# Optimization experiments

Measured on AMD Instinct MI355X. Metric: run time of the kernel, lower is better.

Reference implementation:

```python
import jax, jax.numpy as jnp
import numpy as np

HEADS = 8; KVH = 4; HD = 64; MULT = 2; DIFF = 1; DIM = 512; K = 3
LAMBDA_INIT = 0.2          # 0.8 - 0.6*exp(-0.3*layer_idx), layer_idx=0, affine=False
EPS = 1e-8
ROPE_CONST = 10000.0


def conv2d(x, w):
    # SAME padding (=1) for k=3, stride 1, zeros padding mode, no bias
    return jax.lax.conv_general_dilated(x, w, (1, 1), [(1, 1), (1, 1)],
                                        dimension_numbers=('NCHW', 'OIHW', 'NCHW'))


def rope(x):
    # x: [B, S, h, D]; rotate interleaved pairs (torch view_as_complex layout)
    D = x.shape[-1]; S = x.shape[1]
    theta = 1.0 / (ROPE_CONST ** (jnp.arange(0, D, 2, dtype=jnp.float32) / D))
    ang = jnp.arange(S, dtype=jnp.float32)[:, None] * theta[None, :]      # [S, D/2]
    cos = jnp.cos(ang)[None, :, None, :]
    sin = jnp.sin(ang)[None, :, None, :]
    xr = x.reshape(*x.shape[:-1], D // 2, 2)
    x0, x1 = xr[..., 0], xr[..., 1]
    out = jnp.stack([x0 * cos - x1 * sin, x0 * sin + x1 * cos], axis=-1)
    return out.reshape(x.shape)


def setup_inputs() -> dict:
    key = jax.random.key(0)
    ks = jax.random.split(key, 10)
    conv_std = 1.0 / np.sqrt(DIM * K * K)
    x = jax.random.normal(ks[0], (1, 2, DIM, 64, 64), jnp.float32)
    cross = jax.random.normal(ks[1], (1, 2, DIM, 32, 32), jnp.float32)
    wq = jax.random.normal(ks[2], (HEADS * HD * MULT, DIM, K, K), jnp.float32) * conv_std
    wk = jax.random.normal(ks[3], (KVH * HD * MULT, DIM, K, K), jnp.float32) * conv_std
    wv = jax.random.normal(ks[4], (KVH * HD, DIM, K, K), jnp.float32) * conv_std
    wo = jax.random.normal(ks[5], (DIM, DIM, K, K), jnp.float32) * conv_std
    # lambda params scaled to keep exp(sum over head_dim) numerically sane
    lam_q1 = jax.random.normal(ks[6], (HEADS, HD, DIFF), jnp.float32) * 0.05
    lam_q2 = jax.random.normal(ks[7], (HEADS, HD, DIFF), jnp.float32) * 0.05
    lam_k1 = jax.random.normal(ks[8], (HEADS, HD, DIFF), jnp.float32) * 0.05
    lam_k2 = jax.random.normal(ks[9], (HEADS, HD, DIFF), jnp.float32) * 0.05
    return {'x': x, 'cross': cross, 'wq': wq, 'wk': wk, 'wv': wv, 'wo': wo,
            'lam_q1': lam_q1, 'lam_q2': lam_q2, 'lam_k1': lam_k1, 'lam_k2': lam_k2}


def reference(x, cross, wq, wk, wv, wo, lam_q1, lam_q2, lam_k1, lam_k2):
    g, b, c, H, W = x.shape
    _, _, _, Hc, Wc = cross.shape
    B = g * b; Sq = H * W; Sk = Hc * Wc
    xb = x.reshape(B, c, H, W)
    cb = cross.reshape(B, c, Hc, Wc)
    # conv QKV projections
    q = conv2d(xb, wq)                     # [B, heads*HD*MULT, H, W]
    k = conv2d(cb, wk)                     # [B, KVH*HD*MULT, Hc, Wc]
    v = conv2d(cb, wv)                     # [B, KVH*HD, Hc, Wc]
    # convert: channels are head-major -> [B, S, heads, HD*mult]
    q = q.reshape(B, HEADS, HD * MULT, Sq).transpose(0, 3, 1, 2)
    k = k.reshape(B, KVH, HD * MULT, Sk).transpose(0, 3, 1, 2)
    v = v.reshape(B, KVH, HD, Sk).transpose(0, 3, 1, 2)
    # RoPE over flattened pixel positions, rotating full HD*MULT per head
    q = rope(q)
    k = rope(k)
    # grouped-query: repeat kv heads
    rep = HEADS // KVH
    k = jnp.repeat(k, rep, axis=2)         # [B, Sk, heads, HD*MULT]
    v = jnp.repeat(v, rep, axis=2)         # [B, Sk, heads, HD]
    # split into 1+DIFF score components
    qm = q.reshape(B, Sq, HEADS, MULT, HD)
    km = k.reshape(B, Sk, HEADS, MULT, HD)
    scale = 1.0 / np.sqrt(HD)
    scores = jnp.einsum('bqhmd,bkhmd->bhmqk', qm, km) * scale
    attn = jax.nn.softmax(scores, axis=-1)               # [B, h, MULT, Sq, Sk]
    # differential lambda: ((exp(sum q1*k1) - exp(sum q2*k2)) + init) * (-1)^i
    signs = (-1.0) ** jnp.arange(1, DIFF + 1, dtype=jnp.float32)   # [DIFF]
    lam = (jnp.exp(jnp.sum(lam_q1 * lam_k1, axis=-2))
           - jnp.exp(jnp.sum(lam_q2 * lam_k2, axis=-2)) + LAMBDA_INIT) * signs  # [h, DIFF]
    combined = attn[:, :, 0] + jnp.einsum('hm,bhmqk->bhqk', lam, attn[:, :, 1:])
    out = jnp.einsum('bhqk,bkhd->bqhd', combined, v)     # [B, Sq, h, HD]
    # per-head RMSNorm (affine=False) then post-attention shift
    out = out * jax.lax.rsqrt(jnp.mean(out * out, axis=-1, keepdims=True) + EPS)
    out = out * (1.0 - LAMBDA_INIT)
    # revert to image layout and output conv
    out = out.reshape(B, Sq, HEADS * HD).transpose(0, 2, 1).reshape(B, c, H, W)
    out = conv2d(out, wo)
    return out.reshape(g, b, c, H, W)
```

## Files before the change

### kernel.cpp

```cpp
#include <hip/hip_runtime.h>


typedef __attribute__((ext_vector_type(8))) short short8;
typedef __attribute__((ext_vector_type(4))) float f32x4;
typedef unsigned short us;

__device__ __forceinline__ float bf2f(us u) {
  union { unsigned int i; float f; } v; v.i = ((unsigned int)u) << 16; return v.f;
}
__device__ __forceinline__ us f2bf(float f) {
  union { float f; unsigned int i; } v; v.f = f;
  unsigned int x = v.i;
  return (us)((x + 0x7fffu + ((x >> 16) & 1u)) >> 16);
}

typedef __attribute__((address_space(3))) unsigned int as3_uint;
typedef const __attribute__((address_space(1))) unsigned int as1_uint;
__device__ __forceinline__ void gload16(const us* g, us* l) {
  __builtin_amdgcn_global_load_lds((as1_uint*)g, (as3_uint*)l, 16, 0, 0);
}
__device__ __forceinline__ unsigned int cvt_pk_bf16(float a, float b) {
  unsigned int r;
  asm("v_cvt_pk_bf16_f32 %0, %1, %2" : "=v"(r) : "v"(a), "v"(b));
  return r;
}
__device__ __forceinline__ float fast_exp2(float x) {
  float r;
  asm("v_exp_f32 %0, %1" : "=v"(r) : "v"(x));
  return r;
}
__device__ __forceinline__ void fsincos(float ang, float* sn, float* cs) {
  float r = ang * 0.15915494309f;
  r = r - floorf(r);
  float s, c;
  asm("v_sin_f32 %0, %1" : "=v"(s) : "v"(r));
  asm("v_cos_f32 %0, %1" : "=v"(c) : "v"(r));
  *sn = s; *cs = c;
}

__device__ __forceinline__ void transpose_body(
    const float* __restrict__ in, us* __restrict__ outT,
    int b, int y, int ci0, int H, int W, int logW) {
  const int C = 512;
  int padW = W + 2, Ppad = (H + 2) * padW;
  __shared__ float tile[64][65];
  int nt = W * 64;
  for (int idx = threadIdx.x; idx < nt; idx += 256) {
    int ci = idx >> logW, x = idx & (W - 1);
    tile[ci][x] = in[(((size_t)b * C + ci0 + ci) * H + y) * W + x];
  }
  __syncthreads();
  int nt2 = W * 32;
  for (int idx = threadIdx.x; idx < nt2; idx += 256) {
    int px = idx >> 5, c2 = idx & 31;
    unsigned int val = (unsigned int)f2bf(tile[c2 * 2][px]) |
                       ((unsigned int)f2bf(tile[c2 * 2 + 1][px]) << 16);
    *(unsigned int*)(outT + ((size_t)b * Ppad + (size_t)(y + 1) * padW + (px + 1)) * C +
                     ci0 + c2 * 2) = val;
  }
}

__global__ __launch_bounds__(256) void prep_all(
    const float* __restrict__ x, const float* __restrict__ cross,
    const float* __restrict__ wq, const float* __restrict__ wk,
    const float* __restrict__ wv, const float* __restrict__ wo,
    const float* __restrict__ lq1, const float* __restrict__ lq2,
    const float* __restrict__ lk1, const float* __restrict__ lk2,
    us* __restrict__ xpadT, us* __restrict__ cpadT, us* __restrict__ apad,
    us* __restrict__ oq, us* __restrict__ ok, us* __restrict__ ov,
    us* __restrict__ oo, float* __restrict__ lam) {
  int bid = blockIdx.x, tid = threadIdx.x;
  if (bid < 326) {
    int g = bid * 4 + (tid >> 6);
    int t = tid & 63;
    us* base; int W, b, i;
    if (g < 520)      { base = xpadT; W = 64; b = g >= 260; i = g - b * 260; }
    else if (g < 784) { base = cpadT; W = 32; int gg = g - 520; b = gg >= 132; i = gg - b * 132; }
    else              { base = apad; W = 64; int gg = g - 784; b = gg >= 260; i = gg - b * 260; }
    int padW = W + 2, nb = 2 * padW;
    int yy, xx;
    if (i < padW)    { yy = 0; xx = i; }
    else if (i < nb) { yy = W + 1; xx = i - padW; }
    else             { int j = i - nb; yy = 1 + (j >> 1); xx = (j & 1) * (W + 1); }
    size_t p = ((size_t)b * padW * padW + (size_t)yy * padW + xx) * 512 + t * 8;
    *(int4*)(base + p) = make_int4(0, 0, 0, 0);
  } else if (bid < 1350) {
    int i = bid - 326;
    transpose_body(x, xpadT, i >> 9, (i >> 3) & 63, (i & 7) * 64, 64, 64, 6);
  } else if (bid < 1862) {
    int i = bid - 1350;
    transpose_body(cross, cpadT, i >> 8, (i >> 3) & 31, (i & 7) * 64, 32, 32, 5);
  } else if (bid < 4166) {
    int blk = bid - 1862;
    const float* src; us* dst; int Cout, co;
    if (blk < 1024)      { src = wq; dst = oq; Cout = 1024; co = blk; }
    else if (blk < 1536) { src = wk; dst = ok; Cout = 512;  co = blk - 1024; }
    else if (blk < 1792) { src = wv; dst = ov; Cout = 256;  co = blk - 1536; }
    else                 { src = wo; dst = oo; Cout = 512;  co = blk - 1792; }
    __shared__ us l[4608];
    const float* s0 = src + (size_t)co * 4608;
#pragma unroll
    for (int k = 0; k < 18; ++k) { int i = k * 256 + tid; l[i] = f2bf(s0[i]); }
    __syncthreads();
#pragma unroll
    for (int k = 0; k < 9; ++k) {
      int j = k * 256 + tid;
      int t = j >> 8, c2 = j & 255;
      unsigned int val = (unsigned int)l[(c2 * 2) * 9 + t] |
                         ((unsigned int)l[(c2 * 2 + 1) * 9 + t] << 16);
      *(unsigned int*)(dst + (size_t)t * Cout * 512 + (size_t)co * 512 + c2 * 2) = val;
    }
  } else {
    int h = tid >> 5, d = tid & 31;
    float s1 = lq1[h * 64 + d] * lk1[h * 64 + d] +
               lq1[h * 64 + d + 32] * lk1[h * 64 + d + 32];
    float s2 = lq2[h * 64 + d] * lk2[h * 64 + d] +
               lq2[h * 64 + d + 32] * lk2[h * 64 + d + 32];
    for (int m = 16; m; m >>= 1) {
      s1 += __shfl_xor(s1, m);
      s2 += __shfl_xor(s2, m);
    }
    if (d == 0) lam[h] = -(expf(s1) - expf(s2) + 0.2f);
  }
}

__global__ __launch_bounds__(256) void conv128_fwd(
    const us* __restrict__ inT, const us* __restrict__ wp,
    us* __restrict__ out, int Cout) {
  __shared__ __align__(16) us sh[2][2][128][64];
  int bid = blockIdx.x;
  int v = (bid & 7) * 64 + (bid >> 3);
  int pxt = v & 31, cot = (v >> 5) & 7, b = v >> 8;
  int p0 = pxt * 128, co0 = cot * 128;
  int tid = threadIdx.x;
  int wave = tid >> 6, lane = tid & 63, l15 = lane & 15, hi4 = lane >> 4;
  int wr = wave >> 1, wc = wave & 1;
  f32x4 acc[4][4];
#pragma unroll
  for (int m = 0; m < 4; ++m)
#pragma unroll
    for (int n = 0; n < 4; ++n) acc[m][n] = (f32x4){0.f, 0.f, 0.f, 0.f};

  int arow[4], brow[4];
#pragma unroll
  for (int c = 0; c < 4; ++c) {
    int row = c * 32 + (tid >> 3);
    int g = (tid & 7) ^ (row & 7);
    int px = p0 + row;
    int y = px >> 6, x = px & 63;
    arow[c] = (y * 66 + x) * 512 + g * 8;
    brow[c] = (co0 + row) * 512 + g * 8;
  }
  int aoff[4][2], boff[4][2];
#pragma unroll
  for (int m = 0; m < 4; ++m)
#pragma unroll
    for (int ks = 0; ks < 2; ++ks) {
      int ra = wr * 64 + m * 16 + l15;
      int rb = wc * 64 + m * 16 + l15;
      aoff[m][ks] = ra * 64 + (((ks * 4 + hi4) ^ (l15 & 7)) * 8);
      boff[m][ks] = rb * 64 + (((ks * 4 + hi4) ^ (l15 & 7)) * 8);
    }
  const us* abase = inT + (size_t)b * 66 * 66 * 512;

  auto stage = [&](int buf, int s) {
    int tn = s >> 3, ci = (s & 7) << 6;
    int ky = (tn * 11) >> 5, kx = tn - ky * 3;
    const us* as = abase + (ky * 66 + kx) * 512 + ci;
    const us* bs = wp + (size_t)tn * Cout * 512 + ci;
    us* la = &sh[buf][0][0][0];
    us* lb = &sh[buf][1][0][0];
#pragma unroll
    for (int c = 0; c < 4; ++c) {
      gload16(as + arow[c], la + c * 2048 + wave * 512);
      gload16(bs + brow[c], lb + c * 2048 + wave * 512);
    }
  };

  stage(0, 0);
  __syncthreads();
  for (int s = 0; s < 72; ++s) {
    int cur = s & 1;
    if (s < 71) stage(cur ^ 1, s + 1);
    const us* la = &sh[cur][0][0][0];
    const us* lb = &sh[cur][1][0][0];
#pragma unroll
    for (int ks = 0; ks < 2; ++ks) {
      short8 af[4], bf[4];
#pragma unroll
      for (int m = 0; m < 4; ++m) af[m] = *(const short8*)(la + aoff[m][ks]);
#pragma unroll
      for (int n = 0; n < 4; ++n) bf[n] = *(const short8*)(lb + boff[n][ks]);
#pragma unroll
      for (int m = 0; m < 4; ++m)
#pragma unroll
        for (int n = 0; n < 4; ++n)
          acc[m][n] = __builtin_amdgcn_mfma_f32_16x16x32_bf16(af[m], bf[n], acc[m][n], 0, 0, 0);
    }
    __syncthreads();
  }
  int par = lane & 1;
#pragma unroll
  for (int n = 0; n < 4; ++n) {
    int co = co0 + wc * 64 + n * 16 + l15;
    int j = (co & 127) >> 1;
    float th = exp2f(-(float)j * 0.20762050593f);
    float sth, cth;
    fsincos(th, &sth, &cth);
#pragma unroll
    for (int m = 0; m < 4; ++m) {
      int pxb = p0 + wr * 64 + m * 16 + hi4 * 4;
      float s0, c0;
      fsincos((float)pxb * th, &s0, &c0);
#pragma unroll
      for (int r = 0; r < 4; ++r) {
        float xv = acc[m][n][r];
        float ov = __shfl_xor(xv, 1);
        float y = par ? fmaf(ov, s0, xv * c0) : fmaf(xv, c0, -ov * s0);
        out[((size_t)b * 4096 + (pxb + r)) * Cout + co] = f2bf(y);
        float c1 = c0 * cth - s0 * sth;
        s0 = fmaf(c0, sth, s0 * cth);
        c0 = c1;
      }
    }
  }
}

template <int TRANS_OUT, int ROPE>
__device__ __forceinline__ void conv64_body(
    const us* __restrict__ inT, const us* __restrict__ wp,
    us* __restrict__ out, int Cout, int logCoT, int bid, int ngrid, us* sh) {
  int nchunk = ngrid >> 3;
  int v = (bid & 7) * nchunk + (bid >> 3);
  int yt = v & 15;
  int cot = (v >> 4) & ((1 << logCoT) - 1);
  int b = v >> (4 + logCoT);
  int p0 = yt * 64, co0 = cot * 64;
  const int W = 32, logW = 5, padW = 34, HW = 1024;
  int tid = threadIdx.x;
  int wave = tid >> 6, lane = tid & 63, l15 = lane & 15, hi4 = lane >> 4;
  f32x4 acc[4];
#pragma unroll
  for (int i = 0; i < 4; ++i) acc[i] = (f32x4){0.f, 0.f, 0.f, 0.f};

  int arow[2], brow[2];
#pragma unroll
  for (int c = 0; c < 2; ++c) {
    int row = (wave * 2 + c) * 8 + (lane >> 3);
    int g = (lane & 7) ^ (row & 7);
    int px = p0 + row;
    int y = px >> logW, x = px & (W - 1);
    arow[c] = (y * padW + x) * 512 + g * 8;
    brow[c] = (co0 + row) * 512 + g * 8;
  }
  int gb[2];
#pragma unroll
  for (int ks = 0; ks < 2; ++ks) gb[ks] = ((ks * 4 + hi4) ^ (l15 & 7)) * 8;

  const us* abase = inT + (size_t)b * padW * padW * 512;

  auto stage = [&](int buf, int s) {
    int tn = s >> 3, ci = (s & 7) << 6;
    int ky = (tn * 11) >> 5, kx = tn - ky * 3;
    const us* as = abase + (ky * padW + kx) * 512 + ci;
    const us* bs = wp + (size_t)tn * Cout * 512 + ci;
    us* la = sh + buf * 8192;
    us* lb = la + 4096;
#pragma unroll
    for (int c = 0; c < 2; ++c) {
      gload16(as + arow[c], la + (wave * 2 + c) * 512);
      gload16(bs + brow[c], lb + (wave * 2 + c) * 512);
    }
  };

  stage(0, 0);
  __syncthreads();
  for (int s = 0; s < 72; ++s) {
    int cur = s & 1;
    if (s < 71) stage(cur ^ 1, s + 1);
    const us* la = sh + cur * 8192;
    const us* lb = la + 4096;
#pragma unroll
    for (int ks = 0; ks < 2; ++ks) {
      short8 bf = *(const short8*)(lb + (16 * wave + l15) * 64 + gb[ks]);
#pragma unroll
      for (int i = 0; i < 4; ++i) {
        short8 af = *(const short8*)(la + (i * 16 + l15) * 64 + gb[ks]);
        acc[i] = __builtin_amdgcn_mfma_f32_16x16x32_bf16(af, bf, acc[i], 0, 0, 0);
      }
    }
    __syncthreads();
  }
  if (ROPE) {
    int co = co0 + 16 * wave + l15;
    int j = (co & 127) >> 1;
    float th = exp2f(-(float)j * 0.20762050593f);
    float sth, cth;
    fsincos(th, &sth, &cth);
    int par = lane & 1;
#pragma unroll
    for (int i = 0; i < 4; ++i) {
      int pxb = p0 + i * 16 + hi4 * 4;
      float s0, c0;
      fsincos((float)pxb * th, &s0, &c0);
#pragma unroll
      for (int r = 0; r < 4; ++r) {
        float xv = acc[i][r];
        float ov = __shfl_xor(xv, 1);
        float y = par ? fmaf(ov, s0, xv * c0) : fmaf(xv, c0, -ov * s0);
        out[((size_t)b * HW + (pxb + r)) * Cout + co] = f2bf(y);
        float c1 = c0 * cth - s0 * sth;
        s0 = fmaf(c0, sth, s0 * cth);
        c0 = c1;
      }
    }
  } else {
#pragma unroll
    for (int i = 0; i < 4; ++i)
#pragma unroll
      for (int r = 0; r < 4; ++r) {
        int px = TRANS_OUT ? (p0 + (hi4 * 4 + r) * 4 + i)
                           : (p0 + i * 16 + hi4 * 4 + r);
        int co = co0 + 16 * wave + l15;
        us val = f2bf(acc[i][r]);
        if (TRANS_OUT)
          out[((size_t)b * Cout + co) * HW + px] = val;
        else
          out[((size_t)b * HW + px) * Cout + co] = val;
      }
  }
}

__global__ __launch_bounds__(256) void conv64_all(
    const us* __restrict__ cpadT, const us* __restrict__ wkp,
    const us* __restrict__ wvp, us* __restrict__ kb, us* __restrict__ vT) {
  __shared__ __align__(16) us sh[2][2][64][64];
  int bid = blockIdx.x;
  if (bid < 256) conv64_body<0, 1>(cpadT, wkp, kb, 512, 3, bid, 256, &sh[0][0][0][0]);
  else           conv64_body<1, 0>(cpadT, wvp, vT, 256, 2, bid - 256, 128, &sh[0][0][0][0]);
}

__global__ __launch_bounds__(256) void conv128_out(
    const us* __restrict__ apad, const us* __restrict__ wp,
    float* __restrict__ out) {
  __shared__ __align__(16) us lds[2][12288];
  int bid = blockIdx.x;
  int v = (bid & 7) * 64 + (bid >> 3);
  int pxt = v & 63, cot = (v >> 6) & 3, b = v >> 8;
  int p0 = pxt * 64, co0 = cot * 128;
  int tid = threadIdx.x;
  int wave = tid >> 6, lane = tid & 63, l15 = lane & 15, hi4 = lane >> 4;
  int wr = wave >> 1, wc = wave & 1;
  f32x4 acc[4][2];
#pragma unroll
  for (int m = 0; m < 4; ++m)
#pragma unroll
    for (int n = 0; n < 2; ++n) acc[m][n] = (f32x4){0.f, 0.f, 0.f, 0.f};

  int arow[4], brow[2];
#pragma unroll
  for (int c = 0; c < 4; ++c) {
    int row = c * 32 + (tid >> 3);
    int g = (tid & 7) ^ (row & 7);
    arow[c] = (co0 + row) * 512 + g * 8;
  }
#pragma unroll
  for (int c = 0; c < 2; ++c) {
    int row = c * 32 + (tid >> 3);
    int g = (tid & 7) ^ (row & 7);
    int px = p0 + row;
    int y = px >> 6, x = px & 63;
    brow[c] = (y * 66 + x) * 512 + g * 8;
  }
  int aoff[4][2], boff[2][2];
#pragma unroll
  for (int m = 0; m < 4; ++m)
#pragma unroll
    for (int ks = 0; ks < 2; ++ks) {
      int ra = wr * 64 + m * 16 + l15;
      aoff[m][ks] = ra * 64 + (((ks * 4 + hi4) ^ (l15 & 7)) * 8);
    }
#pragma unroll
  for (int n = 0; n < 2; ++n)
#pragma unroll
    for (int ks = 0; ks < 2; ++ks) {
      int rb = wc * 32 + n * 16 + l15;
      boff[n][ks] = rb * 64 + (((ks * 4 + hi4) ^ (l15 & 7)) * 8);
    }
  const us* bbase = apad + (size_t)b * 4356 * 512;

  auto stage = [&](int buf, int s) {
    int tn = s >> 3, ci = (s & 7) << 6;
    int ky = (tn * 11) >> 5, kx = tn - ky * 3;
    const us* as = wp + (size_t)tn * 512 * 512 + ci;
    const us* bs = bbase + (ky * 66 + kx) * 512 + ci;
    us* la = &lds[buf][0];
    us* lb = la + 8192;
#pragma unroll
    for (int c = 0; c < 4; ++c)
      gload16(as + arow[c], la + c * 2048 + wave * 512);
#pragma unroll
    for (int c = 0; c < 2; ++c)
      gload16(bs + brow[c], lb + c * 2048 + wave * 512);
  };

  stage(0, 0);
  __syncthreads();
  for (int s = 0; s < 72; ++s) {
    int cur = s & 1;
    if (s < 71) stage(cur ^ 1, s + 1);
    const us* la = &lds[cur][0];
    const us* lb = la + 8192;
#pragma unroll
    for (int ks = 0; ks < 2; ++ks) {
      short8 af[4], bf[2];
#pragma unroll
      for (int m = 0; m < 4; ++m) af[m] = *(const short8*)(la + aoff[m][ks]);
#pragma unroll
      for (int n = 0; n < 2; ++n) bf[n] = *(const short8*)(lb + boff[n][ks]);
#pragma unroll
      for (int m = 0; m < 4; ++m)
#pragma unroll
        for (int n = 0; n < 2; ++n)
          acc[m][n] = __builtin_amdgcn_mfma_f32_16x16x32_bf16(af[m], bf[n], acc[m][n], 0, 0, 0);
    }
    __syncthreads();
  }
#pragma unroll
  for (int m = 0; m < 4; ++m)
#pragma unroll
    for (int n = 0; n < 2; ++n)
#pragma unroll
      for (int r = 0; r < 4; ++r) {
        int co = co0 + wr * 64 + m * 16 + hi4 * 4 + r;
        int px = p0 + wc * 32 + n * 16 + l15;
        out[((size_t)b * 512 + co) * 4096 + px] = acc[m][n][r];
      }
}

__global__ __launch_bounds__(256) void attn_kernel(
    const us* __restrict__ qb, const us* __restrict__ kb,
    const us* __restrict__ vT, const float* __restrict__ lam,
    us* __restrict__ apad) {
  int qt = blockIdx.x, h = blockIdx.y, b = blockIdx.z;
  int kvh = h >> 1;
  int tid = threadIdx.x;
  int wave = tid >> 6, lane = tid & 63, l15 = lane & 15, hi4 = lane >> 4;
  __shared__ __align__(16) us Klds[2][8192];
  __shared__ __align__(16) us Vlds[2][4096];
  __shared__ __align__(16) us Plds[4][16][72];

  int q0 = qt * 128;
  short8 qf[2][2][2];
  {
    const us* qsrc =
        qb + ((size_t)(b * 4096 + q0 + wave * 32 + l15)) * 1024 + h * 128 + hi4 * 8;
#pragma unroll
    for (int mf = 0; mf < 2; ++mf)
#pragma unroll
      for (int m = 0; m < 2; ++m)
#pragma unroll
        for (int ks = 0; ks < 2; ++ks)
          qf[mf][m][ks] = *(const short8*)(qsrc + mf * 16384 + m * 64 + ks * 32);
  }

  float sumd[2][2][4];
  f32x4 accO[2][2][4];
#pragma unroll
  for (int mf = 0; mf < 2; ++mf)
#pragma unroll
    for (int m = 0; m < 2; ++m)
#pragma unroll
      for (int r = 0; r < 4; ++r) {
        sumd[mf][m][r] = 0.f;
        accO[mf][m][r] = (f32x4){0.f, 0.f, 0.f, 0.f};
      }
  float lamh = lam[h];

  const us* kbase0 = kb + (size_t)b * 524288 + kvh * 128;
  const us* vbase0 = vT + ((size_t)(b * 256 + kvh * 64)) * 1024;
  int krow[4], vrow[2];
#pragma unroll
  for (int c = 0; c < 4; ++c) {
    int row = (wave * 4 + c) * 4 + hi4;
    int g = (l15 & 8) | ((l15 & 7) ^ (row & 7));
    krow[c] = row * 512 + g * 8;
  }
#pragma unroll
  for (int c = 0; c < 2; ++c) {
    int row = (wave * 2 + c) * 8 + (lane >> 3);
    int g = (lane & 7) ^ (row & 7);
    vrow[c] = row * 1024 + g * 8;
  }
  int kg0[2], kg1[2], vg[2];
#pragma unroll
  for (int m = 0; m < 2; ++m) {
    kg0[m] = (m * 8 | (hi4 ^ (l15 & 7))) * 8;
    kg1[m] = (m * 8 | ((4 + hi4) ^ (l15 & 7))) * 8;
  }
#pragma unroll
  for (int ks = 0; ks < 2; ++ks) vg[ks] = ((ks * 4 + hi4) ^ (l15 & 7)) * 8;

  auto stage = [&](int buf, int kt2) {
    const us* kk = kbase0 + (size_t)kt2 * 32768;
    const us* vv = vbase0 + kt2 * 64;
#pragma unroll
    for (int c = 0; c < 4; ++c)
      gload16(kk + krow[c], &Klds[buf][(wave * 4 + c) * 512]);
#pragma unroll
    for (int c = 0; c < 2; ++c)
      gload16(vv + vrow[c], &Vlds[buf][(wave * 2 + c) * 512]);
  };

  const float cexp = 0.18033688f;
  stage(0, 0);
  for (int kt = 0; kt < 16; ++kt) {
    int cur = kt & 1;
    if (kt < 15) {
      stage(cur ^ 1, kt + 1);
      asm volatile("s_waitcnt vmcnt(6)" ::: "memory");
    } else {
      asm volatile("s_waitcnt vmcnt(0)" ::: "memory");
    }
    __builtin_amdgcn_s_barrier();
    __builtin_amdgcn_sched_barrier(0);

    short8 vf[2][4];
#pragma unroll
    for (int ks = 0; ks < 2; ++ks)
#pragma unroll
      for (int nf = 0; nf < 4; ++nf)
        vf[ks][nf] = *(const short8*)&Vlds[cur][(nf * 16 + l15) * 64 + vg[ks]];

#pragma unroll
    for (int m = 0; m < 2; ++m) {
      short8 kf[4][2];
#pragma unroll
      for (int nf = 0; nf < 4; ++nf) {
        kf[nf][0] = *(const short8*)&Klds[cur][(nf * 16 + l15) * 128 + kg0[m]];
        kf[nf][1] = *(const short8*)&Klds[cur][(nf * 16 + l15) * 128 + kg1[m]];
      }
#pragma unroll
      for (int mf = 0; mf < 2; ++mf) {
        f32x4 s[4];
        __builtin_amdgcn_s_setprio(1);
#pragma unroll
        for (int nf = 0; nf < 4; ++nf) {
          f32x4 z = (f32x4){0.f, 0.f, 0.f, 0.f};
          z = __builtin_amdgcn_mfma_f32_16x16x32_bf16(qf[mf][m][0], kf[nf][0], z, 0, 0, 0);
          z = __builtin_amdgcn_mfma_f32_16x16x32_bf16(qf[mf][m][1], kf[nf][1], z, 0, 0, 0);
          s[nf] = z;
        }
        __builtin_amdgcn_s_setprio(0);
#pragma unroll
        for (int r = 0; r < 4; ++r) {
          float p0 = fast_exp2(s[0][r] * cexp);
          float p1 = fast_exp2(s[1][r] * cexp);
          float p2 = fast_exp2(s[2][r] * cexp);
          float p3 = fast_exp2(s[3][r] * cexp);
          sumd[mf][m][r] += (p0 + p1) + (p2 + p3);
          unsigned int w0 = cvt_pk_bf16(p0, p1);
          unsigned int w1 = cvt_pk_bf16(p2, p3);
          *(uint2*)&Plds[wave][hi4 * 4 + r][l15 * 4] = make_uint2(w0, w1);
        }
        __builtin_amdgcn_s_setprio(1);
#pragma unroll
        for (int ks = 0; ks < 2; ++ks) {
          short8 pf = *(const short8*)&Plds[wave][l15][ks * 32 + hi4 * 8];
#pragma unroll
          for (int nf = 0; nf < 4; ++nf)
            accO[mf][m][nf] =
                __builtin_amdgcn_mfma_f32_16x16x32_bf16(pf, vf[ks][nf], accO[mf][m][nf], 0, 0, 0);
        }
        __builtin_amdgcn_s_setprio(0);
      }
    }
    asm volatile("s_waitcnt lgkmcnt(0)" ::: "memory");
    __builtin_amdgcn_s_barrier();
    __builtin_amdgcn_sched_barrier(0);
  }

#pragma unroll
  for (int mf = 0; mf < 2; ++mf)
#pragma unroll
    for (int m = 0; m < 2; ++m)
#pragma unroll
      for (int r = 0; r < 4; ++r) {
        float sx = sumd[mf][m][r];
        sx += __shfl_xor(sx, 1);
        sx += __shfl_xor(sx, 2);
        sx += __shfl_xor(sx, 4);
        sx += __shfl_xor(sx, 8);
        sumd[mf][m][r] = sx;
      }
#pragma unroll
  for (int mf = 0; mf < 2; ++mf)
#pragma unroll
    for (int r = 0; r < 4; ++r) {
      float inv0 = 1.f / sumd[mf][0][r];
      float inv1 = lamh / sumd[mf][1][r];
      float comb[4];
      float ss = 0.f;
#pragma unroll
      for (int nf = 0; nf < 4; ++nf) {
        comb[nf] = accO[mf][0][nf][r] * inv0 + accO[mf][1][nf][r] * inv1;
        ss += comb[nf] * comb[nf];
      }
      ss += __shfl_xor(ss, 1);
      ss += __shfl_xor(ss, 2);
      ss += __shfl_xor(ss, 4);
      ss += __shfl_xor(ss, 8);
      float sc = rsqrtf(ss * (1.f / 64.f) + 1e-8f) * 0.8f;
      int q = q0 + wave * 32 + mf * 16 + hi4 * 4 + r;
      int y = q >> 6, x = q & 63;
      size_t oaddr = ((size_t)b * 4356 + (size_t)(y + 1) * 66 + (x + 1)) * 512 + h * 64;
#pragma unroll
      for (int nf = 0; nf < 4; ++nf) apad[oaddr + nf * 16 + l15] = f2bf(comb[nf] * sc);
    }
}

extern "C" void kernel_launch(void* const* d_in, const int* in_sizes, int n_in,
                              void* d_out, int out_size, void* d_ws, size_t ws_size,
                              hipStream_t stream) {
  const float* x     = (const float*)d_in[0];
  const float* cross = (const float*)d_in[1];
  const float* wq    = (const float*)d_in[2];
  const float* wk    = (const float*)d_in[3];
  const float* wv    = (const float*)d_in[4];
  const float* wo    = (const float*)d_in[5];
  const float* lq1   = (const float*)d_in[6];
  const float* lq2   = (const float*)d_in[7];
  const float* lk1   = (const float*)d_in[8];
  const float* lk2   = (const float*)d_in[9];
  float* out = (float*)d_out;

  char* ws = (char*)d_ws;
  size_t off = 0;
  auto nxt = [&](size_t bytes) { char* p = ws + off; off += bytes; return p; };
  us* xpadT = (us*)nxt(8921088);
  us* cpadT = (us*)nxt(2367488);
  us* apad  = (us*)nxt(8921088);
  us* wqp = (us*)nxt(9437184);
  us* wkp = (us*)nxt(4718592);
  us* wvp = (us*)nxt(2359296);
  us* wop = (us*)nxt(4718592);
  us* qb  = (us*)nxt(16777216);
  us* kb  = (us*)nxt(2097152);
  us* vT  = (us*)nxt(1048576);
  float* lam = (float*)nxt(256);
  (void)ws_size; (void)in_sizes; (void)n_in; (void)out_size;

  prep_all<<<4167, 256, 0, stream>>>(x, cross, wq, wk, wv, wo,
                                     lq1, lq2, lk1, lk2,
                                     xpadT, cpadT, apad, wqp, wkp, wvp, wop, lam);
  conv128_fwd<<<512, 256, 0, stream>>>(xpadT, wqp, qb, 1024);
  conv64_all<<<384, 256, 0, stream>>>(cpadT, wkp, wvp, kb, vT);
  attn_kernel<<<dim3(32, 8, 2), 256, 0, stream>>>(qb, kb, vT, lam, apad);
  conv128_out<<<512, 256, 0, stream>>>(apad, wop, out);
}
```

Before: 260.2 us.

## Reorder conv K-loop channel-major over taps and halve attention query tile

The three implicit-GEMM conv kernels now step through all nine 3x3 taps for one 64-channel chunk before moving to the next chunk, instead of finishing each tap across all channels first. Consecutive stages therefore read nearby spatial windows of the same channels, which should improve cache locality for the input tiles. Separately, the attention kernel processes 64 queries per block instead of 128 and launches twice as many blocks. This raises parallelism and lowers register pressure, but each block reloads the K/V tiles, so K/V traffic doubles.

Measured after the change: 222.6 us, median of 2. 14.4% less time.

```diff
diff --git a/kernel.cpp b/kernel.cpp
--- a/kernel.cpp
+++ b/kernel.cpp
@@ -163,11 +163,10 @@
     }
   const us* abase = inT + (size_t)b * 66 * 66 * 512;
 
-  auto stage = [&](int buf, int s) {
-    int tn = s >> 3, ci = (s & 7) << 6;
-    int ky = (tn * 11) >> 5, kx = tn - ky * 3;
+  auto stage = [&](int buf, int t, int ci) {
+    int ky = (t * 11) >> 5, kx = t - ky * 3;
     const us* as = abase + (ky * 66 + kx) * 512 + ci;
-    const us* bs = wp + (size_t)tn * Cout * 512 + ci;
+    const us* bs = wp + (size_t)t * Cout * 512 + ci;
     us* la = &sh[buf][0][0][0];
     us* lb = &sh[buf][1][0][0];
 #pragma unroll
@@ -177,27 +176,35 @@
     }
   };
 
-  stage(0, 0);
+  stage(0, 0, 0);
   __syncthreads();
-  for (int s = 0; s < 72; ++s) {
-    int cur = s & 1;
-    if (s < 71) stage(cur ^ 1, s + 1);
-    const us* la = &sh[cur][0][0][0];
-    const us* lb = &sh[cur][1][0][0];
-#pragma unroll
-    for (int ks = 0; ks < 2; ++ks) {
-      short8 af[4], bf[4];
-#pragma unroll
-      for (int m = 0; m < 4; ++m) af[m] = *(const short8*)(la + aoff[m][ks]);
-#pragma unroll
-      for (int n = 0; n < 4; ++n) bf[n] = *(const short8*)(lb + boff[n][ks]);
-#pragma unroll
-      for (int m = 0; m < 4; ++m)
-#pragma unroll
-        for (int n = 0; n < 4; ++n)
-          acc[m][n] = __builtin_amdgcn_mfma_f32_16x16x32_bf16(af[m], bf[n], acc[m][n], 0, 0, 0);
-    }
-    __syncthreads();
+  for (int cc = 0; cc < 8; ++cc) {
+#pragma unroll
+    for (int t = 0; t < 9; ++t) {
+      int s = cc * 9 + t;
+      int cur = s & 1;
+      if (s < 71) {
+        int tn = (t == 8) ? 0 : t + 1;
+        int cn = (t == 8) ? (cc + 1) << 6 : cc << 6;
+        stage(cur ^ 1, tn, cn);
+      }
+      const us* la = &sh[cur][0][0][0];
+      const us* lb = &sh[cur][1][0][0];
+#pragma unroll
+      for (int ks = 0; ks < 2; ++ks) {
+        short8 af[4], bf[4];
+#pragma unroll
+        for (int m = 0; m < 4; ++m) af[m] = *(const short8*)(la + aoff[m][ks]);
+#pragma unroll
+        for (int n = 0; n < 4; ++n) bf[n] = *(const short8*)(lb + boff[n][ks]);
+#pragma unroll
+        for (int m = 0; m < 4; ++m)
+#pragma unroll
+          for (int n = 0; n < 4; ++n)
+            acc[m][n] = __builtin_amdgcn_mfma_f32_16x16x32_bf16(af[m], bf[n], acc[m][n], 0, 0, 0);
+      }
+      __syncthreads();
+    }
   }
   int par = lane & 1;
 #pragma unroll
@@ -259,11 +266,10 @@
 
   const us* abase = inT + (size_t)b * padW * padW * 512;
 
-  auto stage = [&](int buf, int s) {
-    int tn = s >> 3, ci = (s & 7) << 6;
-    int ky = (tn * 11) >> 5, kx = tn - ky * 3;
+  auto stage = [&](int buf, int t, int ci) {
+    int ky = (t * 11) >> 5, kx = t - ky * 3;
     const us* as = abase + (ky * padW + kx) * 512 + ci;
-    const us* bs = wp + (size_t)tn * Cout * 512 + ci;
+    const us* bs = wp + (size_t)t * Cout * 512 + ci;
     us* la = sh + buf * 8192;
     us* lb = la + 4096;
 #pragma unroll
@@ -273,23 +279,31 @@
     }
   };
 
-  stage(0, 0);
+  stage(0, 0, 0);
   __syncthreads();
-  for (int s = 0; s < 72; ++s) {
-    int cur = s & 1;
-    if (s < 71) stage(cur ^ 1, s + 1);
-    const us* la = sh + cur * 8192;
-    const us* lb = la + 4096;
-#pragma unroll
-    for (int ks = 0; ks < 2; ++ks) {
-      short8 bf = *(const short8*)(lb + (16 * wave + l15) * 64 + gb[ks]);
-#pragma unroll
-      for (int i = 0; i < 4; ++i) {
-        short8 af = *(const short8*)(la + (i * 16 + l15) * 64 + gb[ks]);
-        acc[i] = __builtin_amdgcn_mfma_f32_16x16x32_bf16(af, bf, acc[i], 0, 0, 0);
-      }
-    }
-    __syncthreads();
+  for (int cc = 0; cc < 8; ++cc) {
+#pragma unroll
+    for (int t = 0; t < 9; ++t) {
+      int s = cc * 9 + t;
+      int cur = s & 1;
+      if (s < 71) {
+        int tn = (t == 8) ? 0 : t + 1;
+        int cn = (t == 8) ? (cc + 1) << 6 : cc << 6;
+        stage(cur ^ 1, tn, cn);
+      }
+      const us* la = sh + cur * 8192;
+      const us* lb = la + 4096;
+#pragma unroll
+      for (int ks = 0; ks < 2; ++ks) {
+        short8 bf = *(const short8*)(lb + (16 * wave + l15) * 64 + gb[ks]);
+#pragma unroll
+        for (int i = 0; i < 4; ++i) {
+          short8 af = *(const short8*)(la + (i * 16 + l15) * 64 + gb[ks]);
+          acc[i] = __builtin_amdgcn_mfma_f32_16x16x32_bf16(af, bf, acc[i], 0, 0, 0);
+        }
+      }
+      __syncthreads();
+    }
   }
   if (ROPE) {
     int co = co0 + 16 * wave + l15;
@@ -389,10 +403,9 @@
     }
   const us* bbase = apad + (size_t)b * 4356 * 512;
 
-  auto stage = [&](int buf, int s) {
-    int tn = s >> 3, ci = (s & 7) << 6;
-    int ky = (tn * 11) >> 5, kx = tn - ky * 3;
-    const us* as = wp + (size_t)tn * 512 * 512 + ci;
+  auto stage = [&](int buf, int t, int ci) {
+    int ky = (t * 11) >> 5, kx = t - ky * 3;
+    const us* as = wp + (size_t)t * 512 * 512 + ci;
     const us* bs = bbase + (ky * 66 + kx) * 512 + ci;
     us* la = &lds[buf][0];
     us* lb = la + 8192;
@@ -404,27 +417,35 @@
       gload16(bs + brow[c], lb + c * 2048 + wave * 512);
   };
 
-  stage(0, 0);
+  stage(0, 0, 0);
   __syncthreads();
-  for (int s = 0; s < 72; ++s) {
-    int cur = s & 1;
-    if (s < 71) stage(cur ^ 1, s + 1);
-    const us* la = &lds[cur][0];
-    const us* lb = la + 8192;
-#pragma unroll
-    for (int ks = 0; ks < 2; ++ks) {
-      short8 af[4], bf[2];
-#pragma unroll
-      for (int m = 0; m < 4; ++m) af[m] = *(const short8*)(la + aoff[m][ks]);
-#pragma unroll
-      for (int n = 0; n < 2; ++n) bf[n] = *(const short8*)(lb + boff[n][ks]);
-#pragma unroll
-      for (int m = 0; m < 4; ++m)
-#pragma unroll
-        for (int n = 0; n < 2; ++n)
-          acc[m][n] = __builtin_amdgcn_mfma_f32_16x16x32_bf16(af[m], bf[n], acc[m][n], 0, 0, 0);
-    }
-    __syncthreads();
+  for (int cc = 0; cc < 8; ++cc) {
+#pragma unroll
+    for (int t = 0; t < 9; ++t) {
+      int s = cc * 9 + t;
+      int cur = s & 1;
+      if (s < 71) {
+        int tn = (t == 8) ? 0 : t + 1;
+        int cn = (t == 8) ? (cc + 1) << 6 : cc << 6;
+        stage(cur ^ 1, tn, cn);
+      }
+      const us* la = &lds[cur][0];
+      const us* lb = la + 8192;
+#pragma unroll
+      for (int ks = 0; ks < 2; ++ks) {
+        short8 af[4], bf[2];
+#pragma unroll
+        for (int m = 0; m < 4; ++m) af[m] = *(const short8*)(la + aoff[m][ks]);
+#pragma unroll
+        for (int n = 0; n < 2; ++n) bf[n] = *(const short8*)(lb + boff[n][ks]);
+#pragma unroll
+        for (int m = 0; m < 4; ++m)
+#pragma unroll
+          for (int n = 0; n < 2; ++n)
+            acc[m][n] = __builtin_amdgcn_mfma_f32_16x16x32_bf16(af[m], bf[n], acc[m][n], 0, 0, 0);
+      }
+      __syncthreads();
+    }
   }
 #pragma unroll
   for (int m = 0; m < 4; ++m)
@@ -450,31 +471,27 @@
   __shared__ __align__(16) us Vlds[2][4096];
   __shared__ __align__(16) us Plds[4][16][72];
 
-  int q0 = qt * 128;
-  short8 qf[2][2][2];
+  int q0 = qt * 64;
+  short8 qf[2][2];
   {
     const us* qsrc =
-        qb + ((size_t)(b * 4096 + q0 + wave * 32 + l15)) * 1024 + h * 128 + hi4 * 8;
-#pragma unroll
-    for (int mf = 0; mf < 2; ++mf)
-#pragma unroll
-      for (int m = 0; m < 2; ++m)
-#pragma unroll
-        for (int ks = 0; ks < 2; ++ks)
-          qf[mf][m][ks] = *(const short8*)(qsrc + mf * 16384 + m * 64 + ks * 32);
-  }
-
-  float sumd[2][2][4];
-  f32x4 accO[2][2][4];
-#pragma unroll
-  for (int mf = 0; mf < 2; ++mf)
+        qb + ((size_t)(b * 4096 + q0 + wave * 16 + l15)) * 1024 + h * 128 + hi4 * 8;
 #pragma unroll
     for (int m = 0; m < 2; ++m)
 #pragma unroll
-      for (int r = 0; r < 4; ++r) {
-        sumd[mf][m][r] = 0.f;
-        accO[mf][m][r] = (f32x4){0.f, 0.f, 0.f, 0.f};
-      }
+      for (int ks = 0; ks < 2; ++ks)
+        qf[m][ks] = *(const short8*)(qsrc + m * 64 + ks * 32);
+  }
+
+  float sumd[2][4];
+  f32x4 accO[2][4];
+#pragma unroll
+  for (int m = 0; m < 2; ++m)
+#pragma unroll
+    for (int r = 0; r < 4; ++r) {
+      sumd[m][r] = 0.f;
+      accO[m][r] = (f32x4){0.f, 0.f, 0.f, 0.f};
+    }
   float lamh = lam[h];
 
   const us* kbase0 = kb + (size_t)b * 524288 + kvh * 128;
@@ -540,40 +557,37 @@
         kf[nf][0] = *(const short8*)&Klds[cur][(nf * 16 + l15) * 128 + kg0[m]];
         kf[nf][1] = *(const short8*)&Klds[cur][(nf * 16 + l15) * 128 + kg1[m]];
       }
-#pragma unroll
-      for (int mf = 0; mf < 2; ++mf) {
-        f32x4 s[4];
-        __builtin_amdgcn_s_setprio(1);
-#pragma unroll
-        for (int nf = 0; nf < 4; ++nf) {
-          f32x4 z = (f32x4){0.f, 0.f, 0.f, 0.f};
-          z = __builtin_amdgcn_mfma_f32_16x16x32_bf16(qf[mf][m][0], kf[nf][0], z, 0, 0, 0);
-          z = __builtin_amdgcn_mfma_f32_16x16x32_bf16(qf[mf][m][1], kf[nf][1], z, 0, 0, 0);
-          s[nf] = z;
-        }
-        __builtin_amdgcn_s_setprio(0);
-#pragma unroll
-        for (int r = 0; r < 4; ++r) {
-          float p0 = fast_exp2(s[0][r] * cexp);
-          float p1 = fast_exp2(s[1][r] * cexp);
-          float p2 = fast_exp2(s[2][r] * cexp);
-          float p3 = fast_exp2(s[3][r] * cexp);
-          sumd[mf][m][r] += (p0 + p1) + (p2 + p3);
-          unsigned int w0 = cvt_pk_bf16(p0, p1);
-          unsigned int w1 = cvt_pk_bf16(p2, p3);
-          *(uint2*)&Plds[wave][hi4 * 4 + r][l15 * 4] = make_uint2(w0, w1);
-        }
-        __builtin_amdgcn_s_setprio(1);
-#pragma unroll
-        for (int ks = 0; ks < 2; ++ks) {
-          short8 pf = *(const short8*)&Plds[wave][l15][ks * 32 + hi4 * 8];
-#pragma unroll
-          for (int nf = 0; nf < 4; ++nf)
-            accO[mf][m][nf] =
-                __builtin_amdgcn_mfma_f32_16x16x32_bf16(pf, vf[ks][nf], accO[mf][m][nf], 0, 0, 0);
-        }
-        __builtin_amdgcn_s_setprio(0);
-      }
+      f32x4 s[4];
+      __builtin_amdgcn_s_setprio(1);
+#pragma unroll
+      for (int nf = 0; nf < 4; ++nf) {
+        f32x4 z = (f32x4){0.f, 0.f, 0.f, 0.f};
+        z = __builtin_amdgcn_mfma_f32_16x16x32_bf16(qf[m][0], kf[nf][0], z, 0, 0, 0);
+        z = __builtin_amdgcn_mfma_f32_16x16x32_bf16(qf[m][1], kf[nf][1], z, 0, 0, 0);
+        s[nf] = z;
+      }
+      __builtin_amdgcn_s_setprio(0);
+#pragma unroll
+      for (int r = 0; r < 4; ++r) {
+        float p0 = fast_exp2(s[0][r] * cexp);
+        float p1 = fast_exp2(s[1][r] * cexp);
+        float p2 = fast_exp2(s[2][r] * cexp);
+        float p3 = fast_exp2(s[3][r] * cexp);
+        sumd[m][r] += (p0 + p1) + (p2 + p3);
+        unsigned int w0 = cvt_pk_bf16(p0, p1);
+        unsigned int w1 = cvt_pk_bf16(p2, p3);
+        *(uint2*)&Plds[wave][hi4 * 4 + r][l15 * 4] = make_uint2(w0, w1);
+      }
+      __builtin_amdgcn_s_setprio(1);
+#pragma unroll
+      for (int ks = 0; ks < 2; ++ks) {
+        short8 pf = *(const short8*)&Plds[wave][l15][ks * 32 + hi4 * 8];
+#pragma unroll
+        for (int nf = 0; nf < 4; ++nf)
+          accO[m][nf] =
+              __builtin_amdgcn_mfma_f32_16x16x32_bf16(pf, vf[ks][nf], accO[m][nf], 0, 0, 0);
+      }
+      __builtin_amdgcn_s_setprio(0);
     }
     asm volatile("s_waitcnt lgkmcnt(0)" ::: "memory");
     __builtin_amdgcn_s_barrier();
@@ -581,42 +595,38 @@
   }
 
 #pragma unroll
-  for (int mf = 0; mf < 2; ++mf)
-#pragma unroll
-    for (int m = 0; m < 2; ++m)
-#pragma unroll
-      for (int r = 0; r < 4; ++r) {
-        float sx = sumd[mf][m][r];
-        sx += __shfl_xor(sx, 1);
-        sx += __shfl_xor(sx, 2);
-        sx += __shfl_xor(sx, 4);
-        sx += __shfl_xor(sx, 8);
-        sumd[mf][m][r] = sx;
-      }
-#pragma unroll
-  for (int mf = 0; mf < 2; ++mf)
+  for (int m = 0; m < 2; ++m)
 #pragma unroll
     for (int r = 0; r < 4; ++r) {
-      float inv0 = 1.f / sumd[mf][0][r];
-      float inv1 = lamh / sumd[mf][1][r];
-      float comb[4];
-      float ss = 0.f;
-#pragma unroll
-      for (int nf = 0; nf < 4; ++nf) {
-        comb[nf] = accO[mf][0][nf][r] * inv0 + accO[mf][1][nf][r] * inv1;
-        ss += comb[nf] * comb[nf];
-      }
-      ss += __shfl_xor(ss, 1);
-      ss += __shfl_xor(ss, 2);
-      ss += __shfl_xor(ss, 4);
-      ss += __shfl_xor(ss, 8);
-      float sc = rsqrtf(ss * (1.f / 64.f) + 1e-8f) * 0.8f;
-      int q = q0 + wave * 32 + mf * 16 + hi4 * 4 + r;
-      int y = q >> 6, x = q & 63;
-      size_t oaddr = ((size_t)b * 4356 + (size_t)(y + 1) * 66 + (x + 1)) * 512 + h * 64;
-#pragma unroll
-      for (int nf = 0; nf < 4; ++nf) apad[oaddr + nf * 16 + l15] = f2bf(comb[nf] * sc);
-    }
+      float sx = sumd[m][r];
+      sx += __shfl_xor(sx, 1);
+      sx += __shfl_xor(sx, 2);
+      sx += __shfl_xor(sx, 4);
+      sx += __shfl_xor(sx, 8);
+      sumd[m][r] = sx;
+    }
+#pragma unroll
+  for (int r = 0; r < 4; ++r) {
+    float inv0 = 1.f / sumd[0][r];
+    float inv1 = lamh / sumd[1][r];
+    float comb[4];
+    float ss = 0.f;
+#pragma unroll
+    for (int nf = 0; nf < 4; ++nf) {
+      comb[nf] = accO[0][nf][r] * inv0 + accO[1][nf][r] * inv1;
+      ss += comb[nf] * comb[nf];
+    }
+    ss += __shfl_xor(ss, 1);
+    ss += __shfl_xor(ss, 2);
+    ss += __shfl_xor(ss, 4);
+    ss += __shfl_xor(ss, 8);
+    float sc = rsqrtf(ss * (1.f / 64.f) + 1e-8f) * 0.8f;
+    int q = q0 + wave * 16 + hi4 * 4 + r;
+    int y = q >> 6, x = q & 63;
+    size_t oaddr = ((size_t)b * 4356 + (size_t)(y + 1) * 66 + (x + 1)) * 512 + h * 64;
+#pragma unroll
+    for (int nf = 0; nf < 4; ++nf) apad[oaddr + nf * 16 + l15] = f2bf(comb[nf] * sc);
+  }
 }
 
 extern "C" void kernel_launch(void* const* d_in, const int* in_sizes, int n_in,
@@ -655,6 +665,6 @@
                                      xpadT, cpadT, apad, wqp, wkp, wvp, wop, lam);
   conv128_fwd<<<512, 256, 0, stream>>>(xpadT, wqp, qb, 1024);
   conv64_all<<<384, 256, 0, stream>>>(cpadT, wkp, wvp, kb, vT);
-  attn_kernel<<<dim3(32, 8, 2), 256, 0, stream>>>(qb, kb, vT, lam, apad);
+  attn_kernel<<<dim3(64, 8, 2), 256, 0, stream>>>(qb, kb, vT, lam, apad);
   conv128_out<<<512, 256, 0, stream>>>(apad, wop, out);
 }
```
